# Kernel optimization log

Measured on AMD Instinct MI355X. Metric: run time of the kernel, lower is better.

## Reference

```python
import jax, jax.numpy as jnp
import numpy as np

D_MODEL = 1024
N_HEADS = 16
HEAD_DIM = D_MODEL // N_HEADS


def setup_inputs() -> dict:
    key = jax.random.key(0)
    k1, k2, k3, k4, k5 = jax.random.split(key, 5)
    s = 0.02
    return {
        "x": jax.random.normal(k1, (2, 2048, D_MODEL), dtype=jnp.float32),
        "w_qkv": jax.random.normal(k2, (D_MODEL, 3 * D_MODEL), dtype=jnp.float32) * s,
        "b_qkv": jax.random.normal(k3, (3 * D_MODEL,), dtype=jnp.float32) * s,
        "w_proj": jax.random.normal(k4, (D_MODEL, D_MODEL), dtype=jnp.float32) * s,
        "b_proj": jax.random.normal(k5, (D_MODEL,), dtype=jnp.float32) * s,
    }


def reference(x, w_qkv, b_qkv, w_proj, b_proj):
    B, T, C = x.shape
    # fused qkv projection: [B,T,3C] -> [3,B,H,T,Dh]
    qkv = x @ w_qkv + b_qkv
    qkv = qkv.reshape(B, T, 3, N_HEADS, HEAD_DIM).transpose(2, 0, 3, 1, 4)
    q, k, v = qkv[0], qkv[1], qkv[2]
    scale = 1.0 / np.sqrt(HEAD_DIM).astype(np.float32)
    att = jnp.einsum("bhtd,bhsd->bhts", q, k) * scale  # [B,H,T,T]
    causal = jnp.triu(jnp.ones((T, T), dtype=bool), k=1)
    att = jnp.where(causal, -jnp.inf, att)
    att = jax.nn.softmax(att, axis=-1)
    # dropout is identity in eval / p=0
    out = jnp.einsum("bhts,bhsd->bhtd", att, v)  # [B,H,T,Dh]
    out = out.transpose(0, 2, 1, 3).reshape(B, T, C)
    return out @ w_proj + b_proj
```

## Files before the change

kernel.cpp:

```cpp
#include <hip/hip_runtime.h>
#include <hip/hip_bf16.h>
#include <stdint.h>

#define MROWS 4096
#define DMODEL 1024
#define NQKV 3072
#define TSEQ 2048

typedef __attribute__((ext_vector_type(8))) short short8;
typedef __attribute__((ext_vector_type(4))) short short4v;
typedef __attribute__((ext_vector_type(4))) float floatx4;
typedef unsigned short ushort_t;

#define TILE_ELEMS 4608
#define BH_TILE_STRIDE 147456

#define QSCALE 0.1803368801111204f

static __device__ __forceinline__ unsigned short f2bf(float f) {
    union { float f; unsigned u; } v; v.f = f;
    unsigned r = v.u + 0x7fff + ((v.u >> 16) & 1);
    return (unsigned short)(r >> 16);
}


static __device__ __forceinline__ floatx4 mfma16(short4v a, short4v b, floatx4 c) {
#if defined(__HIP_DEVICE_COMPILE__)
#if __has_builtin(__builtin_amdgcn_mfma_f32_16x16x16bf16_1k)
    return __builtin_amdgcn_mfma_f32_16x16x16bf16_1k(a, b, c, 0, 0, 0);
#else
#error "mfma 16x16x16 bf16 builtin unavailable on device"
#endif
#else
    return c;
#endif
}

static __device__ __forceinline__ unsigned pk2bf(float a, float b) {
    unsigned ua = __float_as_uint(a) + 0x8000u;
    unsigned ub = __float_as_uint(b) + 0x8000u;
#if defined(__HIP_DEVICE_COMPILE__) && __has_builtin(__builtin_amdgcn_perm)
    return __builtin_amdgcn_perm(ub, ua, 0x07060302u);
#else
    return (ua >> 16) | (ub & 0xFFFF0000u);
#endif
}

static __device__ __forceinline__ float exp2_fast(float x) {
#if defined(__HIP_DEVICE_COMPILE__) && __has_builtin(__builtin_amdgcn_exp2f)
    return __builtin_amdgcn_exp2f(x);
#else
    return exp2f(x);
#endif
}

static __device__ __forceinline__ void glds16(const void* g, void* l) {
    __builtin_amdgcn_global_load_lds(
        (const __attribute__((address_space(1))) void*)g,
        (__attribute__((address_space(3))) void*)l, 16, 0, 0);
}

__global__ void cast_f32_bf16(const float* __restrict__ in,
                              ushort_t* __restrict__ out, int n) {
    int i = (blockIdx.x * blockDim.x + threadIdx.x) * 4;
    if (i < n) {
        float4 f = *(const float4*)(in + i);
        ushort4 o;
        o.x = f2bf(f.x); o.y = f2bf(f.y); o.z = f2bf(f.z); o.w = f2bf(f.w);
        *(ushort4*)(out + i) = o;
    }
}

__global__ void transpose_cast(const float* __restrict__ in,
                               ushort_t* __restrict__ out, int R, int C) {
    __shared__ float tile[32][33];
    int c0 = blockIdx.x * 32, r0 = blockIdx.y * 32;
    int tx = threadIdx.x & 31, ty = threadIdx.x >> 5;
    for (int i = 0; i < 4; i++) {
        int r = ty + i * 8;
        tile[r][tx] = in[(size_t)(r0 + r) * C + c0 + tx];
    }
    __syncthreads();
    for (int i = 0; i < 4; i++) {
        int r = ty + i * 8;
        out[(size_t)(c0 + r) * R + r0 + tx] = f2bf(tile[tx][r]);
    }
}

__global__ void transpose_v(const ushort_t* __restrict__ in,
                            ushort_t* __restrict__ out) {
    __shared__ ushort_t T[64][72];
    int tile = blockIdx.x, bh = blockIdx.y;
    int tid = threadIdx.x;
    int row = tid >> 2, q4 = tid & 3;
    const ushort_t* ip = in + ((size_t)bh * TSEQ + tile * 64) * 64;
#pragma unroll
    for (int p = 0; p < 2; p++) {
        int c = q4 * 16 + p * 8;
        *(uint4*)(&T[row][c]) = *(const uint4*)(ip + (size_t)row * 64 + c);
    }
    __syncthreads();
    ushort_t* op = out + (size_t)bh * BH_TILE_STRIDE + (size_t)tile * TILE_ELEMS;
#pragma unroll
    for (int p = 0; p < 2; p++) {
        int cbase = q4 * 16 + p * 8;
        ushort_t tmp[8];
#pragma unroll
        for (int e = 0; e < 8; e++) {
            int cp = cbase + e;
            int Q = cp >> 4, SB = (cp >> 2) & 3, J = cp & 3;
            int s = SB * 16 + Q * 4 + J;
            tmp[e] = T[s][row];
        }
        *(uint4*)(op + (size_t)row * 72 + cbase) = *(uint4*)tmp;
    }
}

template <int EPI, int MFRAG>
__global__ __launch_bounds__(256, 2)
void gemm_glds(const ushort_t* __restrict__ A,
               const ushort_t* __restrict__ Bt,
               const float* __restrict__ bias,
               void* __restrict__ out0, void* __restrict__ out1, void* __restrict__ out2,
               int M, int N, int K) {
    __shared__ ushort_t As[2][MFRAG * 1024];
    __shared__ ushort_t Bs[2][4096];
    int tid = threadIdx.x;
    int wave = tid >> 6, lane = tid & 63;
    int quad = lane >> 4, l16 = lane & 15;
    int m0 = blockIdx.y * (MFRAG * 32), n0 = blockIdx.x * 128;
    int wm = (wave & 1) * (MFRAG * 16), wn = (wave >> 1) * 64;

    const floatx4 zero = {0.f, 0.f, 0.f, 0.f};
    floatx4 acc[MFRAG][4];
#pragma unroll
    for (int i = 0; i < MFRAG; i++)
#pragma unroll
        for (int j = 0; j < 4; j++) acc[i][j] = zero;

    int srow = tid >> 2, sc = tid & 3;
    const ushort_t* ag = A  + (size_t)(m0 + srow) * K + sc * 8;
    const ushort_t* bg = Bt + (size_t)(n0 + srow) * K + sc * 8;

    for (int k0 = 0; k0 < K; k0 += 64) {
#pragma unroll
        for (int h2 = 0; h2 < 2; h2++) {
            int kk = k0 + h2 * 32;
            ushort_t* asw = &As[h2][wave * 512];
            ushort_t* bsw = &Bs[h2][wave * 512];
            glds16(ag + kk, asw);
            if (MFRAG == 4) glds16(ag + (size_t)64 * K + kk, asw + 2048);
            glds16(bg + kk, bsw);
            glds16(bg + (size_t)64 * K + kk, bsw + 2048);
        }
        __syncthreads();
#pragma unroll
        for (int h2 = 0; h2 < 2; h2++) {
            short8 af[MFRAG], bf[4];
#pragma unroll
            for (int i = 0; i < MFRAG; i++)
                af[i] = *(const short8*)(&As[h2][(wm + i * 16 + l16) * 32 + quad * 8]);
#pragma unroll
            for (int j = 0; j < 4; j++)
                bf[j] = *(const short8*)(&Bs[h2][(wn + j * 16 + l16) * 32 + quad * 8]);
#pragma unroll
            for (int i = 0; i < MFRAG; i++)
#pragma unroll
                for (int j = 0; j < 4; j++)
                    acc[i][j] = __builtin_amdgcn_mfma_f32_16x16x32_bf16(
                        af[i], bf[j], acc[i][j], 0, 0, 0);
        }
        __syncthreads();
    }

    int sec = n0 >> 10;
    ushort_t* dst = (ushort_t*)(sec == 0 ? out0 : (sec == 1 ? out1 : out2));
#pragma unroll
    for (int i = 0; i < MFRAG; i++) {
        int row = m0 + wm + i * 16 + quad * 4;
#pragma unroll
        for (int j = 0; j < 4; j++) {
            int col = n0 + wn + j * 16 + l16;
            float bvs = bias[col];
#pragma unroll
            for (int r = 0; r < 4; r++) {
                float v = acc[i][j][r] + bvs;
                int rowr = row + r;
                if (EPI == 0) {
                    ((float*)out0)[(size_t)rowr * N + col] = v;
                } else {
                    int b = rowr >> 11, t = rowr & 2047;
                    int within = col & 1023, h = within >> 6, d = within & 63;
                    size_t bh = (size_t)(b * 16 + h);
                    if (sec == 0)
                        dst[(bh * 2048 + t) * 64 + d] = f2bf(v * QSCALE);
                    else if (sec == 1)
                        dst[bh * BH_TILE_STRIDE + (size_t)(t >> 6) * TILE_ELEMS
                            + (size_t)(t & 63) * 72 + d] = f2bf(v);
                    else
                        dst[(bh * 2048 + t) * 64 + d] = f2bf(v);
                }
            }
        }
    }
}

__global__ __launch_bounds__(256, 1)
void attn_kernel(const ushort_t* __restrict__ Qb,
                 const ushort_t* __restrict__ Kt,
                 const ushort_t* __restrict__ Vt,
                 ushort_t* __restrict__ outb) {
    __shared__ ushort_t Ks[2][64 * 72];
    __shared__ ushort_t Vs[2][64 * 72];
    int tid = threadIdx.x;
    int wave = tid >> 6, lane = tid & 63;
    int quad = lane >> 4, l16 = lane & 15;
    int pair = blockIdx.x;
    int bh = blockIdx.y;
    int b = bh >> 4, h = bh & 15;
    const ushort_t* qh = Qb + (size_t)bh * TSEQ * 64;
    const ushort_t* kh = Kt + (size_t)bh * BH_TILE_STRIDE;
    const ushort_t* vh = Vt + (size_t)bh * BH_TILE_STRIDE;
    const floatx4 zero = {0.f, 0.f, 0.f, 0.f};
    int lo8 = lane * 8;

    for (int half = 0; half < 2; half++) {
        int qt = half ? (31 - pair) : pair;
        int q0 = qt * 64;
        int nsteps = qt + 1;

        int qrow = q0 + wave * 16 + l16;
        short8 qf0 = *(const short8*)(qh + (size_t)qrow * 64 + quad * 8);
        short8 qf1 = *(const short8*)(qh + (size_t)qrow * 64 + 32 + quad * 8);

        floatx4 Oacc[4];
#pragma unroll
        for (int j = 0; j < 4; j++) Oacc[j] = zero;
        float lsum = 0.f;

#pragma unroll
        for (int c = 0; c < 3; c++) {
            int cc = wave + 4 * c;
            if (cc < 9) {
                glds16(kh + cc * 512 + lo8, &Ks[0][cc * 512]);
                glds16(vh + cc * 512 + lo8, &Vs[0][cc * 512]);
            }
        }

        for (int step = 0; step < nsteps; step++) {
            int cur = step & 1;
            __syncthreads();
            if (step + 1 < nsteps) {
                const ushort_t* kt = kh + (size_t)(step + 1) * TILE_ELEMS;
                const ushort_t* vt = vh + (size_t)(step + 1) * TILE_ELEMS;
#pragma unroll
                for (int c = 0; c < 3; c++) {
                    int cc = wave + 4 * c;
                    if (cc < 9) {
                        glds16(kt + cc * 512 + lo8, &Ks[cur ^ 1][cc * 512]);
                        glds16(vt + cc * 512 + lo8, &Vs[cur ^ 1][cc * 512]);
                    }
                }
            }
            const ushort_t* ks = &Ks[cur][0];
            const ushort_t* vs = &Vs[cur][0];

            floatx4 S[4];
#pragma unroll
            for (int sb = 0; sb < 4; sb++) {
                short8 kf0 = *(const short8*)(ks + (sb * 16 + l16) * 72 + quad * 8);
                short8 kf1 = *(const short8*)(ks + (sb * 16 + l16) * 72 + 32 + quad * 8);
                floatx4 s = zero;
                s = __builtin_amdgcn_mfma_f32_16x16x32_bf16(kf0, qf0, s, 0, 0, 0);
                s = __builtin_amdgcn_mfma_f32_16x16x32_bf16(kf1, qf1, s, 0, 0, 0);
                S[sb] = s;
            }
            if (step == nsteps - 1) {
                int ql = wave * 16 + l16;
#pragma unroll
                for (int sb = 0; sb < 4; sb++)
#pragma unroll
                    for (int r = 0; r < 4; r++)
                        if (sb * 16 + quad * 4 + r > ql) S[sb][r] = -1e30f;
            }
            float sum = 0.f;
#pragma unroll
            for (int sb = 0; sb < 4; sb++)
#pragma unroll
                for (int r = 0; r < 4; r++) {
                    float p = exp2_fast(S[sb][r]);
                    S[sb][r] = p;
                    sum += p;
                }
            lsum += sum;

            short4v pf[4];
#pragma unroll
            for (int sb = 0; sb < 4; sb++) {
                union { unsigned u[2]; short4v v; } pk;
                pk.u[0] = pk2bf(S[sb][0], S[sb][1]);
                pk.u[1] = pk2bf(S[sb][2], S[sb][3]);
                pf[sb] = pk.v;
            }
#pragma unroll
            for (int jd = 0; jd < 4; jd++) {
                const ushort_t* vrow = vs + (jd * 16 + l16) * 72 + quad * 16;
                short8 vA = *(const short8*)(vrow);
                short8 vB = *(const short8*)(vrow + 8);
                short4v v0 = __builtin_shufflevector(vA, vA, 0, 1, 2, 3);
                short4v v1 = __builtin_shufflevector(vA, vA, 4, 5, 6, 7);
                short4v v2 = __builtin_shufflevector(vB, vB, 0, 1, 2, 3);
                short4v v3 = __builtin_shufflevector(vB, vB, 4, 5, 6, 7);
                Oacc[jd] = mfma16(v0, pf[0], Oacc[jd]);
                Oacc[jd] = mfma16(v1, pf[1], Oacc[jd]);
                Oacc[jd] = mfma16(v2, pf[2], Oacc[jd]);
                Oacc[jd] = mfma16(v3, pf[3], Oacc[jd]);
            }
        }
        {
            float l = lsum;
            l += __shfl_xor(l, 16);
            l += __shfl_xor(l, 32);
            float rl = 1.0f / l;
            int row = b * TSEQ + q0 + wave * 16 + l16;
#pragma unroll
            for (int jd = 0; jd < 4; jd++) {
                int col = h * 64 + jd * 16 + quad * 4;
                ushort4 o;
                o.x = f2bf(Oacc[jd][0] * rl);
                o.y = f2bf(Oacc[jd][1] * rl);
                o.z = f2bf(Oacc[jd][2] * rl);
                o.w = f2bf(Oacc[jd][3] * rl);
                *(ushort4*)(outb + (size_t)row * DMODEL + col) = o;
            }
        }
        __syncthreads();
    }
}

extern "C" void kernel_launch(void* const* d_in, const int* in_sizes, int n_in,
                              void* d_out, int out_size, void* d_ws, size_t ws_size,
                              hipStream_t stream) {
    const float* x      = (const float*)d_in[0];
    const float* w_qkv  = (const float*)d_in[1];
    const float* b_qkv  = (const float*)d_in[2];
    const float* w_proj = (const float*)d_in[3];
    const float* b_proj = (const float*)d_in[4];
    float* out = (float*)d_out;
    char* ws = (char*)d_ws;

    ushort_t* xb     = (ushort_t*)(ws);
    ushort_t* Vt     = (ushort_t*)(ws);
    ushort_t* wqkvT  = (ushort_t*)(ws + 8388608);
    ushort_t* wprojT = (ushort_t*)(ws + 10485760);
    ushort_t* Qb     = (ushort_t*)(ws + 14680064);
    ushort_t* Kt     = (ushort_t*)(ws + 23068672);
    ushort_t* Vb     = (ushort_t*)(ws + 32505856);
    ushort_t* attnb  = Vb;

    cast_f32_bf16<<<4096, 256, 0, stream>>>(x, xb, MROWS * DMODEL);
    transpose_cast<<<dim3(NQKV / 32, DMODEL / 32), 256, 0, stream>>>(w_qkv, wqkvT, DMODEL, NQKV);

    gemm_glds<1, 4><<<dim3(NQKV / 128, MROWS / 128), 256, 0, stream>>>(
        xb, wqkvT, b_qkv, Qb, Kt, Vb, MROWS, NQKV, DMODEL);

    transpose_v<<<dim3(32, 32), 256, 0, stream>>>(Vb, Vt);
    transpose_cast<<<dim3(DMODEL / 32, DMODEL / 32), 256, 0, stream>>>(w_proj, wprojT, DMODEL, DMODEL);

    attn_kernel<<<dim3(16, 32), 256, 0, stream>>>(Qb, Kt, Vt, attnb);

    gemm_glds<0, 2><<<dim3(DMODEL / 128, MROWS / 64), 256, 0, stream>>>(
        attnb, wprojT, b_proj, out, nullptr, nullptr, MROWS, DMODEL, DMODEL);
}
```

Measured before the change: 196.3 us.

## Process 128-key tiles per attention step and single-buffer 32-deep GEMM K loop

```diff
diff --git a/kernel.cpp b/kernel.cpp
--- a/kernel.cpp
+++ b/kernel.cpp
@@ -13,6 +13,7 @@
 typedef unsigned short ushort_t;
 
 #define TILE_ELEMS 4608
+#define STEP_ELEMS 9216
 #define BH_TILE_STRIDE 147456
 
 #define QSCALE 0.1803368801111204f
@@ -123,8 +124,8 @@
                const float* __restrict__ bias,
                void* __restrict__ out0, void* __restrict__ out1, void* __restrict__ out2,
                int M, int N, int K) {
-    __shared__ ushort_t As[2][MFRAG * 1024];
-    __shared__ ushort_t Bs[2][4096];
+    __shared__ ushort_t As[MFRAG * 32 * 32];
+    __shared__ ushort_t Bs[128 * 32];
     int tid = threadIdx.x;
     int wave = tid >> 6, lane = tid & 63;
     int quad = lane >> 4, l16 = lane & 15;
@@ -141,35 +142,28 @@
     int srow = tid >> 2, sc = tid & 3;
     const ushort_t* ag = A  + (size_t)(m0 + srow) * K + sc * 8;
     const ushort_t* bg = Bt + (size_t)(n0 + srow) * K + sc * 8;
-
-    for (int k0 = 0; k0 < K; k0 += 64) {
-#pragma unroll
-        for (int h2 = 0; h2 < 2; h2++) {
-            int kk = k0 + h2 * 32;
-            ushort_t* asw = &As[h2][wave * 512];
-            ushort_t* bsw = &Bs[h2][wave * 512];
-            glds16(ag + kk, asw);
-            if (MFRAG == 4) glds16(ag + (size_t)64 * K + kk, asw + 2048);
-            glds16(bg + kk, bsw);
-            glds16(bg + (size_t)64 * K + kk, bsw + 2048);
-        }
+    ushort_t* asw = As + wave * 512;
+    ushort_t* bsw = Bs + wave * 512;
+
+    for (int k0 = 0; k0 < K; k0 += 32) {
+        glds16(ag + k0, asw);
+        if (MFRAG == 4) glds16(ag + (size_t)64 * K + k0, asw + 2048);
+        glds16(bg + k0, bsw);
+        glds16(bg + (size_t)64 * K + k0, bsw + 2048);
         __syncthreads();
-#pragma unroll
-        for (int h2 = 0; h2 < 2; h2++) {
-            short8 af[MFRAG], bf[4];
-#pragma unroll
-            for (int i = 0; i < MFRAG; i++)
-                af[i] = *(const short8*)(&As[h2][(wm + i * 16 + l16) * 32 + quad * 8]);
+        short8 af[MFRAG], bf[4];
+#pragma unroll
+        for (int i = 0; i < MFRAG; i++)
+            af[i] = *(const short8*)(As + (wm + i * 16 + l16) * 32 + quad * 8);
+#pragma unroll
+        for (int j = 0; j < 4; j++)
+            bf[j] = *(const short8*)(Bs + (wn + j * 16 + l16) * 32 + quad * 8);
+#pragma unroll
+        for (int i = 0; i < MFRAG; i++)
 #pragma unroll
             for (int j = 0; j < 4; j++)
-                bf[j] = *(const short8*)(&Bs[h2][(wn + j * 16 + l16) * 32 + quad * 8]);
-#pragma unroll
-            for (int i = 0; i < MFRAG; i++)
-#pragma unroll
-                for (int j = 0; j < 4; j++)
-                    acc[i][j] = __builtin_amdgcn_mfma_f32_16x16x32_bf16(
-                        af[i], bf[j], acc[i][j], 0, 0, 0);
-        }
+                acc[i][j] = __builtin_amdgcn_mfma_f32_16x16x32_bf16(
+                    af[i], bf[j], acc[i][j], 0, 0, 0);
         __syncthreads();
     }
 
@@ -210,8 +204,8 @@
                  const ushort_t* __restrict__ Kt,
                  const ushort_t* __restrict__ Vt,
                  ushort_t* __restrict__ outb) {
-    __shared__ ushort_t Ks[2][64 * 72];
-    __shared__ ushort_t Vs[2][64 * 72];
+    __shared__ ushort_t Ks[2][128 * 72];
+    __shared__ ushort_t Vs[2][128 * 72];
     int tid = threadIdx.x;
     int wave = tid >> 6, lane = tid & 63;
     int quad = lane >> 4, l16 = lane & 15;
@@ -227,7 +221,7 @@
     for (int half = 0; half < 2; half++) {
         int qt = half ? (31 - pair) : pair;
         int q0 = qt * 64;
-        int nsteps = qt + 1;
+        int nsteps = (qt + 2) >> 1;
 
         int qrow = q0 + wave * 16 + l16;
         short8 qf0 = *(const short8*)(qh + (size_t)qrow * 64 + quad * 8);
@@ -239,9 +233,9 @@
         float lsum = 0.f;
 
 #pragma unroll
-        for (int c = 0; c < 3; c++) {
+        for (int c = 0; c < 5; c++) {
             int cc = wave + 4 * c;
-            if (cc < 9) {
+            if (cc < 18) {
                 glds16(kh + cc * 512 + lo8, &Ks[0][cc * 512]);
                 glds16(vh + cc * 512 + lo8, &Vs[0][cc * 512]);
             }
@@ -251,12 +245,12 @@
             int cur = step & 1;
             __syncthreads();
             if (step + 1 < nsteps) {
-                const ushort_t* kt = kh + (size_t)(step + 1) * TILE_ELEMS;
-                const ushort_t* vt = vh + (size_t)(step + 1) * TILE_ELEMS;
-#pragma unroll
-                for (int c = 0; c < 3; c++) {
+                const ushort_t* kt = kh + (size_t)(step + 1) * STEP_ELEMS;
+                const ushort_t* vt = vh + (size_t)(step + 1) * STEP_ELEMS;
+#pragma unroll
+                for (int c = 0; c < 5; c++) {
                     int cc = wave + 4 * c;
-                    if (cc < 9) {
+                    if (cc < 18) {
                         glds16(kt + cc * 512 + lo8, &Ks[cur ^ 1][cc * 512]);
                         glds16(vt + cc * 512 + lo8, &Vs[cur ^ 1][cc * 512]);
                     }
@@ -265,9 +259,9 @@
             const ushort_t* ks = &Ks[cur][0];
             const ushort_t* vs = &Vs[cur][0];
 
-            floatx4 S[4];
-#pragma unroll
-            for (int sb = 0; sb < 4; sb++) {
+            floatx4 S[8];
+#pragma unroll
+            for (int sb = 0; sb < 8; sb++) {
                 short8 kf0 = *(const short8*)(ks + (sb * 16 + l16) * 72 + quad * 8);
                 short8 kf1 = *(const short8*)(ks + (sb * 16 + l16) * 72 + 32 + quad * 8);
                 floatx4 s = zero;
@@ -277,15 +271,16 @@
             }
             if (step == nsteps - 1) {
                 int ql = wave * 16 + l16;
-#pragma unroll
-                for (int sb = 0; sb < 4; sb++)
+                int dq = step * 128 - q0;
+#pragma unroll
+                for (int sb = 0; sb < 8; sb++)
 #pragma unroll
                     for (int r = 0; r < 4; r++)
-                        if (sb * 16 + quad * 4 + r > ql) S[sb][r] = -1e30f;
+                        if (dq + sb * 16 + quad * 4 + r > ql) S[sb][r] = -1e30f;
             }
             float sum = 0.f;
 #pragma unroll
-            for (int sb = 0; sb < 4; sb++)
+            for (int sb = 0; sb < 8; sb++)
 #pragma unroll
                 for (int r = 0; r < 4; r++) {
                     float p = exp2_fast(S[sb][r]);
@@ -294,9 +289,9 @@
                 }
             lsum += sum;
 
-            short4v pf[4];
-#pragma unroll
-            for (int sb = 0; sb < 4; sb++) {
+            short4v pf[8];
+#pragma unroll
+            for (int sb = 0; sb < 8; sb++) {
                 union { unsigned u[2]; short4v v; } pk;
                 pk.u[0] = pk2bf(S[sb][0], S[sb][1]);
                 pk.u[1] = pk2bf(S[sb][2], S[sb][3]);
@@ -304,17 +299,20 @@
             }
 #pragma unroll
             for (int jd = 0; jd < 4; jd++) {
-                const ushort_t* vrow = vs + (jd * 16 + l16) * 72 + quad * 16;
-                short8 vA = *(const short8*)(vrow);
-                short8 vB = *(const short8*)(vrow + 8);
-                short4v v0 = __builtin_shufflevector(vA, vA, 0, 1, 2, 3);
-                short4v v1 = __builtin_shufflevector(vA, vA, 4, 5, 6, 7);
-                short4v v2 = __builtin_shufflevector(vB, vB, 0, 1, 2, 3);
-                short4v v3 = __builtin_shufflevector(vB, vB, 4, 5, 6, 7);
-                Oacc[jd] = mfma16(v0, pf[0], Oacc[jd]);
-                Oacc[jd] = mfma16(v1, pf[1], Oacc[jd]);
-                Oacc[jd] = mfma16(v2, pf[2], Oacc[jd]);
-                Oacc[jd] = mfma16(v3, pf[3], Oacc[jd]);
+                const ushort_t* vr0 = vs + (jd * 16 + l16) * 72 + quad * 16;
+                const ushort_t* vr1 = vr0 + 64 * 72;
+                short8 vA = *(const short8*)(vr0);
+                short8 vB = *(const short8*)(vr0 + 8);
+                short8 vC = *(const short8*)(vr1);
+                short8 vD = *(const short8*)(vr1 + 8);
+                Oacc[jd] = mfma16(__builtin_shufflevector(vA, vA, 0, 1, 2, 3), pf[0], Oacc[jd]);
+                Oacc[jd] = mfma16(__builtin_shufflevector(vA, vA, 4, 5, 6, 7), pf[1], Oacc[jd]);
+                Oacc[jd] = mfma16(__builtin_shufflevector(vB, vB, 0, 1, 2, 3), pf[2], Oacc[jd]);
+                Oacc[jd] = mfma16(__builtin_shufflevector(vB, vB, 4, 5, 6, 7), pf[3], Oacc[jd]);
+                Oacc[jd] = mfma16(__builtin_shufflevector(vC, vC, 0, 1, 2, 3), pf[4], Oacc[jd]);
+                Oacc[jd] = mfma16(__builtin_shufflevector(vC, vC, 4, 5, 6, 7), pf[5], Oacc[jd]);
+                Oacc[jd] = mfma16(__builtin_shufflevector(vD, vD, 0, 1, 2, 3), pf[6], Oacc[jd]);
+                Oacc[jd] = mfma16(__builtin_shufflevector(vD, vD, 4, 5, 6, 7), pf[7], Oacc[jd]);
             }
         }
         {
```

After: 198.9 us. About the same (+1.3%).

## Remap GEMM blocks per XCD and shrink LDS stage to raise occupancy

Applied to the files above, without the earlier changes.

```diff
diff --git a/kernel.cpp b/kernel.cpp
--- a/kernel.cpp
+++ b/kernel.cpp
@@ -116,19 +116,23 @@
     }
 }
 
-template <int EPI, int MFRAG>
-__global__ __launch_bounds__(256, 2)
+template <int EPI, int MFRAG, int PERXCD>
+__global__ __launch_bounds__(256, 3)
 void gemm_glds(const ushort_t* __restrict__ A,
                const ushort_t* __restrict__ Bt,
                const float* __restrict__ bias,
                void* __restrict__ out0, void* __restrict__ out1, void* __restrict__ out2,
                int M, int N, int K) {
-    __shared__ ushort_t As[2][MFRAG * 1024];
-    __shared__ ushort_t Bs[2][4096];
+    __shared__ ushort_t As[MFRAG * 32 * 32];
+    __shared__ ushort_t Bs[128 * 32];
     int tid = threadIdx.x;
     int wave = tid >> 6, lane = tid & 63;
     int quad = lane >> 4, l16 = lane & 15;
-    int m0 = blockIdx.y * (MFRAG * 32), n0 = blockIdx.x * 128;
+    int id = blockIdx.x;
+    int xcd = id & 7, sidx = id >> 3;
+    int m_idx = xcd * PERXCD + (sidx & (PERXCD - 1));
+    int n_idx = sidx / PERXCD;
+    int m0 = m_idx * (MFRAG * 32), n0 = n_idx * 128;
     int wm = (wave & 1) * (MFRAG * 16), wn = (wave >> 1) * 64;
 
     const floatx4 zero = {0.f, 0.f, 0.f, 0.f};
@@ -141,35 +145,28 @@
     int srow = tid >> 2, sc = tid & 3;
     const ushort_t* ag = A  + (size_t)(m0 + srow) * K + sc * 8;
     const ushort_t* bg = Bt + (size_t)(n0 + srow) * K + sc * 8;
-
-    for (int k0 = 0; k0 < K; k0 += 64) {
-#pragma unroll
-        for (int h2 = 0; h2 < 2; h2++) {
-            int kk = k0 + h2 * 32;
-            ushort_t* asw = &As[h2][wave * 512];
-            ushort_t* bsw = &Bs[h2][wave * 512];
-            glds16(ag + kk, asw);
-            if (MFRAG == 4) glds16(ag + (size_t)64 * K + kk, asw + 2048);
-            glds16(bg + kk, bsw);
-            glds16(bg + (size_t)64 * K + kk, bsw + 2048);
-        }
+    ushort_t* asw = As + wave * 512;
+    ushort_t* bsw = Bs + wave * 512;
+
+    for (int k0 = 0; k0 < K; k0 += 32) {
+        glds16(ag + k0, asw);
+        if (MFRAG == 4) glds16(ag + (size_t)64 * K + k0, asw + 2048);
+        glds16(bg + k0, bsw);
+        glds16(bg + (size_t)64 * K + k0, bsw + 2048);
         __syncthreads();
-#pragma unroll
-        for (int h2 = 0; h2 < 2; h2++) {
-            short8 af[MFRAG], bf[4];
-#pragma unroll
-            for (int i = 0; i < MFRAG; i++)
-                af[i] = *(const short8*)(&As[h2][(wm + i * 16 + l16) * 32 + quad * 8]);
+        short8 af[MFRAG], bf[4];
+#pragma unroll
+        for (int i = 0; i < MFRAG; i++)
+            af[i] = *(const short8*)(As + (wm + i * 16 + l16) * 32 + quad * 8);
+#pragma unroll
+        for (int j = 0; j < 4; j++)
+            bf[j] = *(const short8*)(Bs + (wn + j * 16 + l16) * 32 + quad * 8);
+#pragma unroll
+        for (int i = 0; i < MFRAG; i++)
 #pragma unroll
             for (int j = 0; j < 4; j++)
-                bf[j] = *(const short8*)(&Bs[h2][(wn + j * 16 + l16) * 32 + quad * 8]);
-#pragma unroll
-            for (int i = 0; i < MFRAG; i++)
-#pragma unroll
-                for (int j = 0; j < 4; j++)
-                    acc[i][j] = __builtin_amdgcn_mfma_f32_16x16x32_bf16(
-                        af[i], bf[j], acc[i][j], 0, 0, 0);
-        }
+                acc[i][j] = __builtin_amdgcn_mfma_f32_16x16x32_bf16(
+                    af[i], bf[j], acc[i][j], 0, 0, 0);
         __syncthreads();
     }
 
@@ -361,7 +358,7 @@
     cast_f32_bf16<<<4096, 256, 0, stream>>>(x, xb, MROWS * DMODEL);
     transpose_cast<<<dim3(NQKV / 32, DMODEL / 32), 256, 0, stream>>>(w_qkv, wqkvT, DMODEL, NQKV);
 
-    gemm_glds<1, 4><<<dim3(NQKV / 128, MROWS / 128), 256, 0, stream>>>(
+    gemm_glds<1, 4, 4><<<768, 256, 0, stream>>>(
         xb, wqkvT, b_qkv, Qb, Kt, Vb, MROWS, NQKV, DMODEL);
 
     transpose_v<<<dim3(32, 32), 256, 0, stream>>>(Vb, Vt);
@@ -369,6 +366,6 @@
 
     attn_kernel<<<dim3(16, 32), 256, 0, stream>>>(Qb, Kt, Vt, attnb);
 
-    gemm_glds<0, 2><<<dim3(DMODEL / 128, MROWS / 64), 256, 0, stream>>>(
+    gemm_glds<0, 2, 8><<<512, 256, 0, stream>>>(
         attnb, wprojT, b_proj, out, nullptr, nullptr, MROWS, DMODEL, DMODEL);
 }
```

Result: no change. 194.7 us (-0.8%).
